# Performance work log

Hardware: AMD Instinct MI355X
Metric: run time of the kernel (lower is better)

The kernel has to match this reference:

```python
import jax, jax.numpy as jnp
import numpy as np

B, S, DIM, H = 2, 2048, 2048, 16
HD = DIM // H  # head_dim = 128
EPS = 1e-6


def setup_inputs() -> dict:
    key = jax.random.key(0)
    ks = jax.random.split(key, 13)
    d = {
        'hidden_states': jax.random.normal(ks[0], (B, S, DIM), jnp.float32),
        'freqs_cos': jax.random.normal(ks[1], (1, S, 1, HD), jnp.float32),
        'freqs_sin': jax.random.normal(ks[2], (1, S, 1, HD), jnp.float32),
        'Wq': jax.random.normal(ks[3], (DIM, DIM), jnp.float32) * 0.02,
        'bq': jax.random.normal(ks[4], (DIM,), jnp.float32) * 0.02,
        'Wk': jax.random.normal(ks[5], (DIM, DIM), jnp.float32) * 0.02,
        'bk': jax.random.normal(ks[6], (DIM,), jnp.float32) * 0.02,
        'Wv': jax.random.normal(ks[7], (DIM, DIM), jnp.float32) * 0.02,
        'bv': jax.random.normal(ks[8], (DIM,), jnp.float32) * 0.02,
        'norm_q_w': jax.random.uniform(ks[9], (DIM,), jnp.float32, 0.5, 1.5),
        'norm_k_w': jax.random.uniform(ks[10], (DIM,), jnp.float32, 0.5, 1.5),
        'Wo': jax.random.normal(ks[11], (DIM, DIM), jnp.float32) * 0.02,
        'bo': jax.random.normal(ks[12], (DIM,), jnp.float32) * 0.02,
    }
    return d


def _rms_norm(x, w, eps=EPS):
    # local RMSNorm over the full inner_dim (no cross-rank reduce)
    xf = x.astype(jnp.float32)
    var = jnp.mean(xf * xf, axis=-1, keepdims=True)
    return (w * (xf * jax.lax.rsqrt(var + eps))).astype(x.dtype)


def _apply_rope(x, freqs_cos, freqs_sin):
    # x: [B,H,S,D]; freqs: [1,S,1,D] -> broadcast cos/sin at [1,1,S,D/2]
    dtype = x.dtype
    xf = x.astype(jnp.float32)
    x1 = xf[..., 0::2]
    x2 = xf[..., 1::2]
    cos = jnp.transpose(freqs_cos[..., 0::2], (0, 2, 1, 3)).astype(jnp.float32)
    sin = jnp.transpose(freqs_sin[..., 1::2], (0, 2, 1, 3)).astype(jnp.float32)
    even = x1 * cos - x2 * sin
    odd = x1 * sin + x2 * cos
    out = jnp.stack([even, odd], axis=-1).reshape(x.shape)
    return out.astype(dtype)


def reference(hidden_states, freqs_cos, freqs_sin, Wq, bq, Wk, bk, Wv, bv,
              norm_q_w, norm_k_w, Wo, bo):
    b, s, _ = hidden_states.shape
    q = hidden_states @ Wq.T + bq
    k = hidden_states @ Wk.T + bk
    v = hidden_states @ Wv.T + bv
    q = _rms_norm(q, norm_q_w)
    k = _rms_norm(k, norm_k_w)
    # [B,S,H*D] -> [B,H,S,D]
    q = q.reshape(b, s, H, HD).transpose(0, 2, 1, 3)
    k = k.reshape(b, s, H, HD).transpose(0, 2, 1, 3)
    v = v.reshape(b, s, H, HD).transpose(0, 2, 1, 3)
    q = _apply_rope(q, freqs_cos, freqs_sin)
    k = _apply_rope(k, freqs_cos, freqs_sin)
    # flash attention math (full, non-causal), scale = 1/sqrt(head_dim)
    scale = 1.0 / np.sqrt(HD).astype(np.float32)
    scores = jnp.einsum('bhqd,bhkd->bhqk', q, k) * scale
    attn = jax.nn.softmax(scores, axis=-1)
    out = jnp.einsum('bhqk,bhkd->bhqd', attn, v)
    out = out.transpose(0, 2, 1, 3).reshape(b, s, H * HD)
    return out @ Wo.T + bo
```

## Files before the change

kernel.cpp:

```cpp
#include <hip/hip_runtime.h>
#include <stdint.h>

#define DEVI __device__ __forceinline__

typedef __attribute__((ext_vector_type(8))) short bf16x8;
typedef __attribute__((ext_vector_type(4))) float f32x4;
typedef __attribute__((ext_vector_type(16))) float f32x16;
typedef __attribute__((ext_vector_type(4))) unsigned short u16x4;
typedef __attribute__((ext_vector_type(8))) unsigned short u16x8;

DEVI unsigned short f2bf(float f) {
    union { float f; unsigned u; } v; v.f = f;
    unsigned r = v.u + 0x7fffu + ((v.u >> 16) & 1u);
    return (unsigned short)(r >> 16);
}

DEVI unsigned cvtpk(float lo, float hi) {
    unsigned r;
    asm("v_cvt_pk_bf16_f32 %0, %1, %2" : "=v"(r) : "v"(lo), "v"(hi));
    return r;
}

DEVI void gload16(const void* g, void* lds) {
    __builtin_amdgcn_global_load_lds(
        (const __attribute__((address_space(1))) unsigned int*)(uintptr_t)g,
        (__attribute__((address_space(3))) unsigned int*)(unsigned int)(uintptr_t)lds,
        16, 0, 0);
}

__global__ __launch_bounds__(256) void cvt_bf16(const float* __restrict__ in,
                                                unsigned short* __restrict__ out, int n4) {
    int i = blockIdx.x * 256 + threadIdx.x;
    if (i >= n4) return;
    float4 v = ((const float4*)in)[i];
    u16x4 pk;
    pk[0] = f2bf(v.x); pk[1] = f2bf(v.y); pk[2] = f2bf(v.z); pk[3] = f2bf(v.w);
    ((u16x4*)out)[i] = pk;
}

DEVI void gemm_pipe_core(const unsigned short* __restrict__ A,
                         const unsigned short* __restrict__ Wt,
                         int m0, int n0, unsigned short* Al, unsigned short* Bl,
                         f32x16 acc[2][2]) {
    constexpr int K = 2048, NT = 32;
    const int t = threadIdx.x;
    const int w = t >> 6, l = t & 63;
    const int q = l & 31, h = l >> 5;
    const int wr = w >> 2, wc = w & 3;
    const int qx = q & 7;
    const int srow = t >> 3, sseg = (t & 7) ^ (srow & 7);
    const unsigned short* aS = A + (size_t)(m0 + srow) * K + sseg * 8;
    const unsigned short* bS = Wt + (size_t)(n0 + srow) * K + sseg * 8;

#pragma unroll
    for (int mi = 0; mi < 2; mi++)
#pragma unroll
        for (int ni = 0; ni < 2; ni++)
#pragma unroll
            for (int r = 0; r < 16; r++) acc[mi][ni][r] = 0.f;

    auto STAGE_P1 = [&](int rb, int kt) {
        const int k0 = kt * 64;
        char* bd = (char*)Bl + rb * 32768 + w * 1024;
        char* ad = (char*)Al + rb * 16384 + w * 1024;
        gload16(bS + k0, bd);
        gload16(bS + (size_t)64 * K + k0, bd + 8192);
        gload16(aS + k0, ad);
    };
    auto STAGE_P2 = [&](int rb, int kt) {
        const int k0 = kt * 64;
        char* bd = (char*)Bl + rb * 32768 + w * 1024;
        char* ad = (char*)Al + rb * 16384 + w * 1024;
        gload16(bS + (size_t)128 * K + k0, bd + 16384);
        gload16(bS + (size_t)192 * K + k0, bd + 24576);
        gload16(aS + (size_t)64 * K + k0, ad + 8192);
    };

    STAGE_P1(0, 0); STAGE_P2(0, 0);
    STAGE_P1(1, 1); STAGE_P2(1, 1);
    asm volatile("s_waitcnt vmcnt(6)" ::: "memory");
    __builtin_amdgcn_s_barrier();

    int rb = 0;
    for (int kt = 0; kt < NT; ++kt) {
        const int r2 = (rb >= 1) ? rb - 1 : 2;
        const char* Ab = (const char*)Al + rb * 16384;
        const char* Bb = (const char*)Bl + rb * 32768;
        bf16x8 a[2][4], b[4];
#pragma unroll
        for (int mi = 0; mi < 2; mi++)
#pragma unroll
            for (int ks = 0; ks < 4; ks++)
                a[mi][ks] = *(const bf16x8*)(Ab + (wr * 64 + mi * 32 + q) * 128 +
                                             (((ks * 2 + h) ^ qx) << 4));
#pragma unroll
        for (int ks = 0; ks < 4; ks++)
            b[ks] = *(const bf16x8*)(Bb + (wc * 64 + q) * 128 +
                                     (((ks * 2 + h) ^ qx) << 4));
        if (kt + 2 < NT) STAGE_P1(r2, kt + 2);
        __builtin_amdgcn_s_barrier();
        __builtin_amdgcn_s_setprio(1);
#pragma unroll
        for (int ks = 0; ks < 4; ks++) {
            acc[0][0] = __builtin_amdgcn_mfma_f32_32x32x16_bf16(a[0][ks], b[ks], acc[0][0], 0, 0, 0);
            acc[1][0] = __builtin_amdgcn_mfma_f32_32x32x16_bf16(a[1][ks], b[ks], acc[1][0], 0, 0, 0);
        }
        __builtin_amdgcn_s_setprio(0);
        __builtin_amdgcn_s_barrier();
#pragma unroll
        for (int ks = 0; ks < 4; ks++)
            b[ks] = *(const bf16x8*)(Bb + (wc * 64 + 32 + q) * 128 +
                                     (((ks * 2 + h) ^ qx) << 4));
        if (kt + 2 < NT) STAGE_P2(r2, kt + 2);
        __builtin_amdgcn_s_barrier();
        __builtin_amdgcn_s_setprio(1);
#pragma unroll
        for (int ks = 0; ks < 4; ks++) {
            acc[0][1] = __builtin_amdgcn_mfma_f32_32x32x16_bf16(a[0][ks], b[ks], acc[0][1], 0, 0, 0);
            acc[1][1] = __builtin_amdgcn_mfma_f32_32x32x16_bf16(a[1][ks], b[ks], acc[1][1], 0, 0, 0);
        }
        __builtin_amdgcn_s_setprio(0);
        if (kt + 2 < NT) asm volatile("s_waitcnt vmcnt(6)" ::: "memory");
        else             asm volatile("s_waitcnt vmcnt(0)" ::: "memory");
        __builtin_amdgcn_s_barrier();
        rb = (rb + 1 >= 3) ? 0 : rb + 1;
    }
}

__global__ __launch_bounds__(512, 2) void gemm_qkv(
    const unsigned short* __restrict__ A,
    const unsigned short* __restrict__ Wq16, const unsigned short* __restrict__ Wk16,
    const unsigned short* __restrict__ Wv16,
    const float* __restrict__ bq, const float* __restrict__ bk, const float* __restrict__ bv,
    float* __restrict__ qf, float* __restrict__ kf, unsigned short* __restrict__ Vt) {
    __shared__ unsigned short Al[3 * 128 * 64];
    __shared__ unsigned short Bl[3 * 256 * 64];
    const int bid = blockIdx.x;
    const int nt = bid & 7, rem = bid >> 3;
    const int mt = rem / 3, z = rem % 3;
    const int m0 = mt * 128, n0 = nt * 256;
    const unsigned short* W = (z == 0) ? Wq16 : (z == 1) ? Wk16 : Wv16;
    const float* bias = (z == 0) ? bq : (z == 1) ? bk : bv;

    f32x16 acc[2][2];
    gemm_pipe_core(A, W, m0, n0, Al, Bl, acc);

    const int t = threadIdx.x, w = t >> 6, l = t & 63;
    const int q = l & 31, h = l >> 5;
    const int wr = w >> 2, wc = w & 3;
#pragma unroll
    for (int mi = 0; mi < 2; mi++)
#pragma unroll
        for (int ni = 0; ni < 2; ni++) {
            const int col = n0 + wc * 64 + ni * 32 + q;
            const float bb = bias[col];
            if (z == 2) {
                const int hh = col >> 7, d = col & 127;
#pragma unroll
                for (int rq = 0; rq < 4; rq++) {
                    const int row = m0 + wr * 64 + mi * 32 + 8 * rq + 4 * h;
                    const int b = row >> 11, s = row & 2047;
                    u16x4 pk;
#pragma unroll
                    for (int j = 0; j < 4; j++) pk[j] = f2bf(acc[mi][ni][rq * 4 + j] + bb);
                    *(u16x4*)(Vt + ((size_t)((b * 16 + hh) * 128 + d)) * 2048 + s) = pk;
                }
            } else {
                float* out = (z == 0) ? qf : kf;
#pragma unroll
                for (int rq = 0; rq < 4; rq++) {
                    const int row = m0 + wr * 64 + mi * 32 + 8 * rq + 4 * h;
#pragma unroll
                    for (int j = 0; j < 4; j++)
                        out[(size_t)(row + j) * 2048 + col] = acc[mi][ni][rq * 4 + j] + bb;
                }
            }
        }
}

__global__ __launch_bounds__(512, 2) void gemm_o(
    const unsigned short* __restrict__ A, const unsigned short* __restrict__ W16,
    const float* __restrict__ bo, float* __restrict__ out) {
    __shared__ unsigned short Al[3 * 128 * 64];
    __shared__ unsigned short Bl[3 * 256 * 64];
    const int bid = blockIdx.x;
    const int swz = (bid & 7) * 32 + (bid >> 3);
    const int mt = swz >> 3, nt = swz & 7;
    const int m0 = mt * 128, n0 = nt * 256;

    f32x16 acc[2][2];
    gemm_pipe_core(A, W16, m0, n0, Al, Bl, acc);

    const int t = threadIdx.x, w = t >> 6, l = t & 63;
    const int q = l & 31, h = l >> 5;
    const int wr = w >> 2, wc = w & 3;
#pragma unroll
    for (int mi = 0; mi < 2; mi++)
#pragma unroll
        for (int ni = 0; ni < 2; ni++) {
            const int col = n0 + wc * 64 + ni * 32 + q;
            const float bb = bo[col];
#pragma unroll
            for (int rq = 0; rq < 4; rq++) {
                const int row = m0 + wr * 64 + mi * 32 + 8 * rq + 4 * h;
#pragma unroll
                for (int j = 0; j < 4; j++)
                    out[(size_t)(row + j) * 2048 + col] = acc[mi][ni][rq * 4 + j] + bb;
            }
        }
}

__global__ __launch_bounds__(256) void norm_rope(
    const float* __restrict__ qf, const float* __restrict__ kf,
    const float* __restrict__ nqw, const float* __restrict__ nkw,
    const float* __restrict__ fc, const float* __restrict__ fs,
    unsigned short* __restrict__ Qr, unsigned short* __restrict__ Kr) {
    const int row = blockIdx.x;
    const int which = blockIdx.y;
    const float* in = which ? kf : qf;
    const float* wv = which ? nkw : nqw;
    unsigned short* out = which ? Kr : Qr;
    const float qs = which ? 1.0f : 0.12751744f;
    const int t = threadIdx.x;
    const float* x = in + (size_t)row * 2048 + t * 8;
    float4 v0 = ((const float4*)x)[0];
    float4 v1 = ((const float4*)x)[1];
    float xv[8] = {v0.x, v0.y, v0.z, v0.w, v1.x, v1.y, v1.z, v1.w};
    float ss = 0.f;
#pragma unroll
    for (int e = 0; e < 8; e++) ss += xv[e] * xv[e];
#pragma unroll
    for (int m = 1; m < 64; m <<= 1) ss += __shfl_xor(ss, m, 64);
    __shared__ float red[4];
    if ((t & 63) == 0) red[t >> 6] = ss;
    __syncthreads();
    const float tot = red[0] + red[1] + red[2] + red[3];
    const float r = rsqrtf(tot * (1.0f / 2048.0f) + 1e-6f);
    const int s = row & 2047, b = row >> 11;
    const int d0 = t * 8, hd0 = d0 & 127, h = d0 >> 7;
    float4 c0 = ((const float4*)(fc + s * 128 + hd0))[0];
    float4 c1 = ((const float4*)(fc + s * 128 + hd0))[1];
    float4 s0 = ((const float4*)(fs + s * 128 + hd0))[0];
    float4 s1 = ((const float4*)(fs + s * 128 + hd0))[1];
    float4 w0 = ((const float4*)(wv + d0))[0];
    float4 w1 = ((const float4*)(wv + d0))[1];
    float wn[8] = {w0.x, w0.y, w0.z, w0.w, w1.x, w1.y, w1.z, w1.w};
    float xn[8];
#pragma unroll
    for (int e = 0; e < 8; e++) xn[e] = xv[e] * wn[e] * r;
    float o[8];
    o[0] = xn[0] * c0.x - xn[1] * s0.y;  o[1] = xn[0] * s0.y + xn[1] * c0.x;
    o[2] = xn[2] * c0.z - xn[3] * s0.w;  o[3] = xn[2] * s0.w + xn[3] * c0.z;
    o[4] = xn[4] * c1.x - xn[5] * s1.y;  o[5] = xn[4] * s1.y + xn[5] * c1.x;
    o[6] = xn[6] * c1.z - xn[7] * s1.w;  o[7] = xn[6] * s1.w + xn[7] * c1.z;
    u16x8 pk;
#pragma unroll
    for (int e = 0; e < 8; e++) pk[e] = f2bf(o[e] * qs);
    *(u16x8*)(out + ((size_t)((b * 16 + h) * 2048 + s)) * 128 + hd0) = pk;
}

__global__ __launch_bounds__(512, 2) void attn(
    const unsigned short* __restrict__ Qr, const unsigned short* __restrict__ Kr,
    const unsigned short* __restrict__ Vt, unsigned short* __restrict__ Ao) {
    __shared__ unsigned short Kl[2][64 * 128];
    __shared__ unsigned short Vl[2][128 * 64];
    const int t = threadIdx.x, w = t >> 6, l = t & 63;
    const int ql = l & 31, h = l >> 5;
    const int bid = blockIdx.x;
    const int xcd = bid & 7, idx = bid >> 3;
    const int bh = xcd * 4 + (idx >> 3);
    const int q0 = (idx & 7) * 256 + w * 32;
    const int b = bh >> 4, head = bh & 15;

    const unsigned short* Qp = Qr + ((size_t)bh * 2048 + q0) * 128;
    bf16x8 qf[8];
#pragma unroll
    for (int c8 = 0; c8 < 8; c8++)
        qf[c8] = *(const bf16x8*)(Qp + ql * 128 + c8 * 16 + h * 8);

    f32x16 accO[4];
#pragma unroll
    for (int dt = 0; dt < 4; dt++)
#pragma unroll
        for (int r = 0; r < 16; r++) accO[dt][r] = 0.f;
    float mj = -1e30f, ljp = 0.f;

    const unsigned short* Kb = Kr + (size_t)bh * 2048 * 128;
    const unsigned short* Vb = Vt + (size_t)bh * 128 * 2048;
    const int krow = t >> 4, kseg = (t & 15) ^ (krow & 7);
    const int vrow = t >> 3, vseg = (t & 7) ^ (vrow & 7);

    auto STAGE = [&](int buf, int kv0) {
        char* kd = (char*)&Kl[buf][0] + w * 1024;
        char* vd = (char*)&Vl[buf][0] + w * 1024;
        gload16(Kb + (size_t)(kv0 + krow) * 128 + kseg * 8, kd);
        gload16(Kb + (size_t)(kv0 + 32 + krow) * 128 + kseg * 8, kd + 8192);
        gload16(Vb + (size_t)vrow * 2048 + kv0 + vseg * 8, vd);
        gload16(Vb + (size_t)(64 + vrow) * 2048 + kv0 + vseg * 8, vd + 8192);
    };

    const int qx = ql & 7;
    STAGE(0, 0);
    __syncthreads();
    int cur = 0;
    for (int it = 0; it < 32; ++it) {
        if (it < 31) STAGE(cur ^ 1, (it + 1) * 64);
        f32x16 S0, S1;
#pragma unroll
        for (int r = 0; r < 16; r++) { S0[r] = 0.f; S1[r] = 0.f; }
        __builtin_amdgcn_s_setprio(1);
#pragma unroll
        for (int c8 = 0; c8 < 8; c8++) {
            const int sg = ((c8 * 2 + h) ^ qx) << 4;
            bf16x8 k0 = *(const bf16x8*)((const char*)&Kl[cur][0] + ql * 256 + sg);
            bf16x8 k1 = *(const bf16x8*)((const char*)&Kl[cur][0] + (32 + ql) * 256 + sg);
            S0 = __builtin_amdgcn_mfma_f32_32x32x16_bf16(k0, qf[c8], S0, 0, 0, 0);
            S1 = __builtin_amdgcn_mfma_f32_32x32x16_bf16(k1, qf[c8], S1, 0, 0, 0);
        }
        __builtin_amdgcn_s_setprio(0);
        float mloc = S0[0];
#pragma unroll
        for (int r = 1; r < 16; r++) mloc = fmaxf(mloc, S0[r]);
#pragma unroll
        for (int r = 0; r < 16; r++) mloc = fmaxf(mloc, S1[r]);
        const float mx = fmaxf(mloc, __shfl_xor(mloc, 32, 64));
        if (!__all(mx <= mj + 8.0f)) {
            const float mn = fmaxf(mj, mx);
            const float corr = exp2f(mj - mn);
            mj = mn;
            ljp *= corr;
#pragma unroll
            for (int dt = 0; dt < 4; dt++)
#pragma unroll
                for (int r = 0; r < 16; r++) accO[dt][r] *= corr;
        }
        unsigned W[16];
        float lsum = 0.f;
#pragma unroll
        for (int i = 0; i < 8; i++) {
            const float pa = exp2f(S0[2 * i] - mj);
            const float pb = exp2f(S0[2 * i + 1] - mj);
            W[i] = cvtpk(pa, pb);
            lsum += pa + pb;
        }
#pragma unroll
        for (int i = 0; i < 8; i++) {
            const float pa = exp2f(S1[2 * i] - mj);
            const float pb = exp2f(S1[2 * i + 1] - mj);
            W[8 + i] = cvtpk(pa, pb);
            lsum += pa + pb;
        }
        ljp += lsum;
#pragma unroll
        for (int c = 0; c < 2; c++) {
            unsigned X[8];
#pragma unroll
            for (int i = 0; i < 8; i++)
                X[i] = (unsigned)__shfl_xor((int)W[c * 8 + i], 32, 64);
            union U { unsigned u[4]; bf16x8 v; };
            U F, G;
            F.u[0] = h ? X[2] : W[c * 8 + 0];
            F.u[1] = h ? X[3] : W[c * 8 + 1];
            F.u[2] = h ? W[c * 8 + 2] : X[0];
            F.u[3] = h ? W[c * 8 + 3] : X[1];
            G.u[0] = h ? X[6] : W[c * 8 + 4];
            G.u[1] = h ? X[7] : W[c * 8 + 5];
            G.u[2] = h ? W[c * 8 + 6] : X[4];
            G.u[3] = h ? W[c * 8 + 7] : X[5];
            __builtin_amdgcn_s_setprio(1);
#pragma unroll
            for (int dt = 0; dt < 4; dt++) {
                const int sg = (((2 * c) * 2 + h) ^ qx) << 4;
                bf16x8 vf = *(const bf16x8*)((const char*)&Vl[cur][0] + (dt * 32 + ql) * 128 + sg);
                accO[dt] = __builtin_amdgcn_mfma_f32_32x32x16_bf16(vf, F.v, accO[dt], 0, 0, 0);
            }
#pragma unroll
            for (int dt = 0; dt < 4; dt++) {
                const int sg = (((2 * c + 1) * 2 + h) ^ qx) << 4;
                bf16x8 vf = *(const bf16x8*)((const char*)&Vl[cur][0] + (dt * 32 + ql) * 128 + sg);
                accO[dt] = __builtin_amdgcn_mfma_f32_32x32x16_bf16(vf, G.v, accO[dt], 0, 0, 0);
            }
            __builtin_amdgcn_s_setprio(0);
        }
        __syncthreads();
        cur ^= 1;
    }
    const float lj = ljp + __shfl_xor(ljp, 32, 64);
    const float inv = 1.0f / lj;
    unsigned short* ob = Ao + ((size_t)(b * 2048 + q0 + ql)) * 2048 + head * 128;
#pragma unroll
    for (int dt = 0; dt < 4; dt++)
#pragma unroll
        for (int i = 0; i < 8; i++) {
            const float a = accO[dt][2 * i] * inv;
            const float c = accO[dt][2 * i + 1] * inv;
            const int d = dt * 32 + ((2 * i) & 3) + 8 * (i >> 1) + 4 * h;
            *(unsigned*)(ob + d) = cvtpk(a, c);
        }
}

extern "C" void kernel_launch(void* const* d_in, const int* in_sizes, int n_in,
                              void* d_out, int out_size, void* d_ws, size_t ws_size,
                              hipStream_t stream) {
    const float* hs  = (const float*)d_in[0];
    const float* fc  = (const float*)d_in[1];
    const float* fs  = (const float*)d_in[2];
    const float* Wq  = (const float*)d_in[3];
    const float* bq  = (const float*)d_in[4];
    const float* Wk  = (const float*)d_in[5];
    const float* bk  = (const float*)d_in[6];
    const float* Wv  = (const float*)d_in[7];
    const float* bv  = (const float*)d_in[8];
    const float* nqw = (const float*)d_in[9];
    const float* nkw = (const float*)d_in[10];
    const float* Wo  = (const float*)d_in[11];
    const float* bo  = (const float*)d_in[12];
    float* out = (float*)d_out;

    char* p = (char*)d_ws;
    unsigned short* hs16 = (unsigned short*)p; p += (size_t)8388608 * 2;
    unsigned short* Wq16 = (unsigned short*)p; p += (size_t)4194304 * 2;
    unsigned short* Wk16 = (unsigned short*)p; p += (size_t)4194304 * 2;
    unsigned short* Wv16 = (unsigned short*)p; p += (size_t)4194304 * 2;
    unsigned short* Wo16 = (unsigned short*)p; p += (size_t)4194304 * 2;
    float* qf = (float*)p;                     p += (size_t)8388608 * 4;
    float* kf = (float*)p;                     p += (size_t)8388608 * 4;
    unsigned short* Qr = (unsigned short*)p;   p += (size_t)8388608 * 2;
    unsigned short* Kr = (unsigned short*)p;   p += (size_t)8388608 * 2;
    unsigned short* Vt = (unsigned short*)p;   p += (size_t)8388608 * 2;
    unsigned short* Ao = (unsigned short*)p;   p += (size_t)8388608 * 2;
    (void)ws_size; (void)in_sizes; (void)n_in; (void)out_size;

    cvt_bf16<<<8192, 256, 0, stream>>>(hs, hs16, 2097152);
    cvt_bf16<<<4096, 256, 0, stream>>>(Wq, Wq16, 1048576);
    cvt_bf16<<<4096, 256, 0, stream>>>(Wk, Wk16, 1048576);
    cvt_bf16<<<4096, 256, 0, stream>>>(Wv, Wv16, 1048576);
    cvt_bf16<<<4096, 256, 0, stream>>>(Wo, Wo16, 1048576);

    gemm_qkv<<<768, 512, 0, stream>>>(hs16, Wq16, Wk16, Wv16,
                                      bq, bk, bv, qf, kf, Vt);
    norm_rope<<<dim3(4096, 2), 256, 0, stream>>>(qf, kf, nqw, nkw, fc, fs, Qr, Kr);
    attn<<<256, 512, 0, stream>>>(Qr, Kr, Vt, Ao);
    gemm_o<<<256, 512, 0, stream>>>(Ao, Wo16, bo, out);
}
```

Baseline: 334.0 us.

## Rework GEMM core to 16x16x32 MFMA with double-buffered four-phase pipeline

The shared GEMM core moves from 32x32x16 MFMA to 16x16x32 MFMA fragments, and the LDS ring goes from three stages to two. Each k-step is split into four quadrant phases that reuse loaded A/B fragments, with global-to-LDS loads spread across the phases. The gemm_o block swizzle is dropped in favour of a plain row-major tile order. Intent is better overlap of loads with MFMA and less LDS pressure, at the cost of more barriers, a shallower prefetch depth and possibly worse L2 locality in gemm_o.

New measurement: 315.2 us. 5.6% less time.

```diff
diff --git a/kernel.cpp b/kernel.cpp
--- a/kernel.cpp
+++ b/kernel.cpp
@@ -40,90 +40,124 @@
 
 DEVI void gemm_pipe_core(const unsigned short* __restrict__ A,
                          const unsigned short* __restrict__ Wt,
-                         int m0, int n0, unsigned short* Al, unsigned short* Bl,
-                         f32x16 acc[2][2]) {
-    constexpr int K = 2048, NT = 32;
+                         int m0, int n0, char* lds,
+                         f32x4 (&acc)[2][2][2][2]) {
+    constexpr int K = 2048;
     const int t = threadIdx.x;
-    const int w = t >> 6, l = t & 63;
-    const int q = l & 31, h = l >> 5;
+    const int w = t >> 6, l = t & 63, lr = l & 15, lk = l >> 4;
     const int wr = w >> 2, wc = w & 3;
-    const int qx = q & 7;
+    const int sx = lr & 7;
     const int srow = t >> 3, sseg = (t & 7) ^ (srow & 7);
     const unsigned short* aS = A + (size_t)(m0 + srow) * K + sseg * 8;
     const unsigned short* bS = Wt + (size_t)(n0 + srow) * K + sseg * 8;
-
-#pragma unroll
-    for (int mi = 0; mi < 2; mi++)
-#pragma unroll
-        for (int ni = 0; ni < 2; ni++)
-#pragma unroll
-            for (int r = 0; r < 16; r++) acc[mi][ni][r] = 0.f;
-
-    auto STAGE_P1 = [&](int rb, int kt) {
-        const int k0 = kt * 64;
-        char* bd = (char*)Bl + rb * 32768 + w * 1024;
-        char* ad = (char*)Al + rb * 16384 + w * 1024;
-        gload16(bS + k0, bd);
-        gload16(bS + (size_t)64 * K + k0, bd + 8192);
-        gload16(aS + k0, ad);
+    char* Bbase = lds + 32768;
+
+#pragma unroll
+    for (int qm = 0; qm < 2; qm++)
+#pragma unroll
+        for (int qn = 0; qn < 2; qn++)
+#pragma unroll
+            for (int fr = 0; fr < 2; fr++)
+#pragma unroll
+                for (int fc = 0; fc < 2; fc++)
+                    acc[qm][qn][fr][fc] = (f32x4){0.f, 0.f, 0.f, 0.f};
+
+    auto STAGE = [&](int tt, int u) {
+        if (tt >= 32) return;
+        const int k0 = tt * 64, bb = tt & 1;
+        if (u < 4)
+            gload16(bS + (size_t)u * 64 * K + k0, Bbase + bb * 32768 + u * 8192 + w * 1024);
+        else
+            gload16(aS + (size_t)(u - 4) * 64 * K + k0, lds + bb * 16384 + (u - 4) * 8192 + w * 1024);
     };
-    auto STAGE_P2 = [&](int rb, int kt) {
-        const int k0 = kt * 64;
-        char* bd = (char*)Bl + rb * 32768 + w * 1024;
-        char* ad = (char*)Al + rb * 16384 + w * 1024;
-        gload16(bS + (size_t)128 * K + k0, bd + 16384);
-        gload16(bS + (size_t)192 * K + k0, bd + 24576);
-        gload16(aS + (size_t)64 * K + k0, ad + 8192);
-    };
-
-    STAGE_P1(0, 0); STAGE_P2(0, 0);
-    STAGE_P1(1, 1); STAGE_P2(1, 1);
-    asm volatile("s_waitcnt vmcnt(6)" ::: "memory");
+
+    STAGE(0, 0); STAGE(0, 1); STAGE(0, 2); STAGE(0, 3); STAGE(0, 4); STAGE(0, 5);
+    STAGE(1, 0); STAGE(1, 1); STAGE(1, 2);
+    asm volatile("s_waitcnt vmcnt(3)" ::: "memory");
     __builtin_amdgcn_s_barrier();
 
-    int rb = 0;
-    for (int kt = 0; kt < NT; ++kt) {
-        const int r2 = (rb >= 1) ? rb - 1 : 2;
-        const char* Ab = (const char*)Al + rb * 16384;
-        const char* Bb = (const char*)Bl + rb * 32768;
-        bf16x8 a[2][4], b[4];
-#pragma unroll
-        for (int mi = 0; mi < 2; mi++)
-#pragma unroll
-            for (int ks = 0; ks < 4; ks++)
-                a[mi][ks] = *(const bf16x8*)(Ab + (wr * 64 + mi * 32 + q) * 128 +
-                                             (((ks * 2 + h) ^ qx) << 4));
-#pragma unroll
-        for (int ks = 0; ks < 4; ks++)
-            b[ks] = *(const bf16x8*)(Bb + (wc * 64 + q) * 128 +
-                                     (((ks * 2 + h) ^ qx) << 4));
-        if (kt + 2 < NT) STAGE_P1(r2, kt + 2);
+    for (int kt = 0; kt < 32; ++kt) {
+        const int bb = kt & 1;
+        const char* Ab = lds + bb * 16384;
+        const char* Bb = Bbase + bb * 32768;
+        bf16x8 a0[2][2], a1[2][2], b0[2][2], b1[2][2];
+#pragma unroll
+        for (int fr = 0; fr < 2; fr++)
+#pragma unroll
+            for (int ks = 0; ks < 2; ks++)
+                a0[fr][ks] = *(const bf16x8*)(Ab + (wr * 64 + fr * 16 + lr) * 128 +
+                                              (((ks * 4 + lk) ^ sx) << 4));
+#pragma unroll
+        for (int fc = 0; fc < 2; fc++)
+#pragma unroll
+            for (int ks = 0; ks < 2; ks++)
+                b0[fc][ks] = *(const bf16x8*)(Bb + (wc * 64 + fc * 16 + lr) * 128 +
+                                              (((ks * 4 + lk) ^ sx) << 4));
+        STAGE(kt + 1, 3); STAGE(kt + 1, 4);
         __builtin_amdgcn_s_barrier();
         __builtin_amdgcn_s_setprio(1);
 #pragma unroll
-        for (int ks = 0; ks < 4; ks++) {
-            acc[0][0] = __builtin_amdgcn_mfma_f32_32x32x16_bf16(a[0][ks], b[ks], acc[0][0], 0, 0, 0);
-            acc[1][0] = __builtin_amdgcn_mfma_f32_32x32x16_bf16(a[1][ks], b[ks], acc[1][0], 0, 0, 0);
-        }
+        for (int ks = 0; ks < 2; ks++)
+#pragma unroll
+            for (int fr = 0; fr < 2; fr++)
+#pragma unroll
+                for (int fc = 0; fc < 2; fc++)
+                    acc[0][0][fr][fc] = __builtin_amdgcn_mfma_f32_16x16x32_bf16(
+                        a0[fr][ks], b0[fc][ks], acc[0][0][fr][fc], 0, 0, 0);
         __builtin_amdgcn_s_setprio(0);
         __builtin_amdgcn_s_barrier();
 #pragma unroll
-        for (int ks = 0; ks < 4; ks++)
-            b[ks] = *(const bf16x8*)(Bb + (wc * 64 + 32 + q) * 128 +
-                                     (((ks * 2 + h) ^ qx) << 4));
-        if (kt + 2 < NT) STAGE_P2(r2, kt + 2);
+        for (int fc = 0; fc < 2; fc++)
+#pragma unroll
+            for (int ks = 0; ks < 2; ks++)
+                b1[fc][ks] = *(const bf16x8*)(Bb + (wc * 64 + 32 + fc * 16 + lr) * 128 +
+                                              (((ks * 4 + lk) ^ sx) << 4));
+        STAGE(kt + 1, 5);
         __builtin_amdgcn_s_barrier();
         __builtin_amdgcn_s_setprio(1);
 #pragma unroll
-        for (int ks = 0; ks < 4; ks++) {
-            acc[0][1] = __builtin_amdgcn_mfma_f32_32x32x16_bf16(a[0][ks], b[ks], acc[0][1], 0, 0, 0);
-            acc[1][1] = __builtin_amdgcn_mfma_f32_32x32x16_bf16(a[1][ks], b[ks], acc[1][1], 0, 0, 0);
-        }
+        for (int ks = 0; ks < 2; ks++)
+#pragma unroll
+            for (int fr = 0; fr < 2; fr++)
+#pragma unroll
+                for (int fc = 0; fc < 2; fc++)
+                    acc[0][1][fr][fc] = __builtin_amdgcn_mfma_f32_16x16x32_bf16(
+                        a0[fr][ks], b1[fc][ks], acc[0][1][fr][fc], 0, 0, 0);
         __builtin_amdgcn_s_setprio(0);
-        if (kt + 2 < NT) asm volatile("s_waitcnt vmcnt(6)" ::: "memory");
-        else             asm volatile("s_waitcnt vmcnt(0)" ::: "memory");
-        __builtin_amdgcn_s_barrier();
-        rb = (rb + 1 >= 3) ? 0 : rb + 1;
+        __builtin_amdgcn_s_barrier();
+#pragma unroll
+        for (int fr = 0; fr < 2; fr++)
+#pragma unroll
+            for (int ks = 0; ks < 2; ks++)
+                a1[fr][ks] = *(const bf16x8*)(Ab + (wr * 64 + 32 + fr * 16 + lr) * 128 +
+                                              (((ks * 4 + lk) ^ sx) << 4));
+        STAGE(kt + 2, 0); STAGE(kt + 2, 1);
+        __builtin_amdgcn_s_barrier();
+        __builtin_amdgcn_s_setprio(1);
+#pragma unroll
+        for (int ks = 0; ks < 2; ks++)
+#pragma unroll
+            for (int fr = 0; fr < 2; fr++)
+#pragma unroll
+                for (int fc = 0; fc < 2; fc++)
+                    acc[1][1][fr][fc] = __builtin_amdgcn_mfma_f32_16x16x32_bf16(
+                        a1[fr][ks], b1[fc][ks], acc[1][1][fr][fc], 0, 0, 0);
+        __builtin_amdgcn_s_setprio(0);
+        __builtin_amdgcn_s_barrier();
+        STAGE(kt + 2, 2);
+        __builtin_amdgcn_s_setprio(1);
+#pragma unroll
+        for (int ks = 0; ks < 2; ks++)
+#pragma unroll
+            for (int fr = 0; fr < 2; fr++)
+#pragma unroll
+                for (int fc = 0; fc < 2; fc++)
+                    acc[1][0][fr][fc] = __builtin_amdgcn_mfma_f32_16x16x32_bf16(
+                        a1[fr][ks], b0[fc][ks], acc[1][0][fr][fc], 0, 0, 0);
+        __builtin_amdgcn_s_setprio(0);
+        if (kt < 30)       asm volatile("s_waitcnt vmcnt(3)" ::: "memory");
+        else if (kt == 30) asm volatile("s_waitcnt vmcnt(0)" ::: "memory");
+        __builtin_amdgcn_s_barrier();
     }
 }
 
@@ -133,8 +167,7 @@
     const unsigned short* __restrict__ Wv16,
     const float* __restrict__ bq, const float* __restrict__ bk, const float* __restrict__ bv,
     float* __restrict__ qf, float* __restrict__ kf, unsigned short* __restrict__ Vt) {
-    __shared__ unsigned short Al[3 * 128 * 64];
-    __shared__ unsigned short Bl[3 * 256 * 64];
+    __shared__ char Lds[98304];
     const int bid = blockIdx.x;
     const int nt = bid & 7, rem = bid >> 3;
     const int mt = rem / 3, z = rem % 3;
@@ -142,72 +175,66 @@
     const unsigned short* W = (z == 0) ? Wq16 : (z == 1) ? Wk16 : Wv16;
     const float* bias = (z == 0) ? bq : (z == 1) ? bk : bv;
 
-    f32x16 acc[2][2];
-    gemm_pipe_core(A, W, m0, n0, Al, Bl, acc);
-
-    const int t = threadIdx.x, w = t >> 6, l = t & 63;
-    const int q = l & 31, h = l >> 5;
+    f32x4 acc[2][2][2][2];
+    gemm_pipe_core(A, W, m0, n0, Lds, acc);
+
+    const int t = threadIdx.x, w = t >> 6, l = t & 63, lr = l & 15, lk = l >> 4;
     const int wr = w >> 2, wc = w & 3;
 #pragma unroll
-    for (int mi = 0; mi < 2; mi++)
-#pragma unroll
-        for (int ni = 0; ni < 2; ni++) {
-            const int col = n0 + wc * 64 + ni * 32 + q;
-            const float bb = bias[col];
-            if (z == 2) {
-                const int hh = col >> 7, d = col & 127;
-#pragma unroll
-                for (int rq = 0; rq < 4; rq++) {
-                    const int row = m0 + wr * 64 + mi * 32 + 8 * rq + 4 * h;
-                    const int b = row >> 11, s = row & 2047;
-                    u16x4 pk;
-#pragma unroll
-                    for (int j = 0; j < 4; j++) pk[j] = f2bf(acc[mi][ni][rq * 4 + j] + bb);
-                    *(u16x4*)(Vt + ((size_t)((b * 16 + hh) * 128 + d)) * 2048 + s) = pk;
+    for (int qm = 0; qm < 2; qm++)
+#pragma unroll
+        for (int qn = 0; qn < 2; qn++)
+#pragma unroll
+            for (int fr = 0; fr < 2; fr++)
+#pragma unroll
+                for (int fc = 0; fc < 2; fc++) {
+                    const int col = n0 + wc * 64 + qn * 32 + fc * 16 + lr;
+                    const int rb = m0 + wr * 64 + qm * 32 + fr * 16 + lk * 4;
+                    const float bb = bias[col];
+                    if (z == 2) {
+                        const int hh = col >> 7, d = col & 127;
+                        const int b = rb >> 11, s = rb & 2047;
+                        u16x4 pk;
+#pragma unroll
+                        for (int j = 0; j < 4; j++) pk[j] = f2bf(acc[qm][qn][fr][fc][j] + bb);
+                        *(u16x4*)(Vt + ((size_t)((b * 16 + hh) * 128 + d)) * 2048 + s) = pk;
+                    } else {
+                        float* out = (z == 0) ? qf : kf;
+#pragma unroll
+                        for (int j = 0; j < 4; j++)
+                            out[(size_t)(rb + j) * 2048 + col] = acc[qm][qn][fr][fc][j] + bb;
+                    }
                 }
-            } else {
-                float* out = (z == 0) ? qf : kf;
-#pragma unroll
-                for (int rq = 0; rq < 4; rq++) {
-                    const int row = m0 + wr * 64 + mi * 32 + 8 * rq + 4 * h;
-#pragma unroll
-                    for (int j = 0; j < 4; j++)
-                        out[(size_t)(row + j) * 2048 + col] = acc[mi][ni][rq * 4 + j] + bb;
-                }
-            }
-        }
 }
 
 __global__ __launch_bounds__(512, 2) void gemm_o(
     const unsigned short* __restrict__ A, const unsigned short* __restrict__ W16,
     const float* __restrict__ bo, float* __restrict__ out) {
-    __shared__ unsigned short Al[3 * 128 * 64];
-    __shared__ unsigned short Bl[3 * 256 * 64];
+    __shared__ char Lds[98304];
     const int bid = blockIdx.x;
-    const int swz = (bid & 7) * 32 + (bid >> 3);
-    const int mt = swz >> 3, nt = swz & 7;
+    const int nt = bid & 7, mt = bid >> 3;
     const int m0 = mt * 128, n0 = nt * 256;
 
-    f32x16 acc[2][2];
-    gemm_pipe_core(A, W16, m0, n0, Al, Bl, acc);
-
-    const int t = threadIdx.x, w = t >> 6, l = t & 63;
-    const int q = l & 31, h = l >> 5;
+    f32x4 acc[2][2][2][2];
+    gemm_pipe_core(A, W16, m0, n0, Lds, acc);
+
+    const int t = threadIdx.x, w = t >> 6, l = t & 63, lr = l & 15, lk = l >> 4;
     const int wr = w >> 2, wc = w & 3;
 #pragma unroll
-    for (int mi = 0; mi < 2; mi++)
-#pragma unroll
-        for (int ni = 0; ni < 2; ni++) {
-            const int col = n0 + wc * 64 + ni * 32 + q;
-            const float bb = bo[col];
-#pragma unroll
-            for (int rq = 0; rq < 4; rq++) {
-                const int row = m0 + wr * 64 + mi * 32 + 8 * rq + 4 * h;
-#pragma unroll
-                for (int j = 0; j < 4; j++)
-                    out[(size_t)(row + j) * 2048 + col] = acc[mi][ni][rq * 4 + j] + bb;
-            }
-        }
+    for (int qm = 0; qm < 2; qm++)
+#pragma unroll
+        for (int qn = 0; qn < 2; qn++)
+#pragma unroll
+            for (int fr = 0; fr < 2; fr++)
+#pragma unroll
+                for (int fc = 0; fc < 2; fc++) {
+                    const int col = n0 + wc * 64 + qn * 32 + fc * 16 + lr;
+                    const int rb = m0 + wr * 64 + qm * 32 + fr * 16 + lk * 4;
+                    const float bb = bo[col];
+#pragma unroll
+                    for (int j = 0; j < 4; j++)
+                        out[(size_t)(rb + j) * 2048 + col] = acc[qm][qn][fr][fc][j] + bb;
+                }
 }
 
 __global__ __launch_bounds__(256) void norm_rope(
```
